# Kernel optimization log

Measured on AMD Instinct MI355X. Metric: run time of the kernel, lower is better.

The kernel has to match this reference:

```python
import jax, jax.numpy as jnp
import numpy as np

N_NODES = 50000
N_EDGES = 800000
IN_CH = 128
OUT_CH = 64
HEADS = 4
NEG_SLOPE = 0.2  # PyG GATConv default


def setup_inputs() -> dict:
    key = jax.random.key(0)
    k1, k2, k3, k4, k5 = jax.random.split(key, 5)
    x = jax.random.normal(k1, (N_NODES, IN_CH), dtype=jnp.float32)
    edge_index = jax.random.randint(k2, (2, N_EDGES), 0, N_NODES, dtype=jnp.int64)
    W = jax.random.normal(k3, (HEADS * OUT_CH, IN_CH), dtype=jnp.float32) * (1.0 / np.sqrt(IN_CH))
    att_src = jax.random.normal(k4, (HEADS, OUT_CH), dtype=jnp.float32) * (1.0 / np.sqrt(OUT_CH))
    att_dst = jax.random.normal(k5, (HEADS, OUT_CH), dtype=jnp.float32) * (1.0 / np.sqrt(OUT_CH))
    bias = jnp.zeros((OUT_CH,), dtype=jnp.float32)
    return {"x": x, "edge_index": edge_index, "W": W,
            "att_src": att_src, "att_dst": att_dst, "bias": bias}


def reference(x, edge_index, W, att_src, att_dst, bias):
    # GAT2NO_NORM.forward in eval mode: dropout == identity.
    N = x.shape[0]
    H, C = att_src.shape
    # PyG GATConv adds self-loops by default.
    loop = jnp.arange(N, dtype=edge_index.dtype)
    src = jnp.concatenate([edge_index[0], loop])  # message source j
    dst = jnp.concatenate([edge_index[1], loop])  # message target i
    # Linear projection, reshape to heads: [N, H, C]
    h = (x @ W.T).reshape(N, H, C)
    # Per-node attention halves: [N, H]
    a_src = jnp.einsum('nhc,hc->nh', h, att_src)
    a_dst = jnp.einsum('nhc,hc->nh', h, att_dst)
    # Per-edge raw score, LeakyReLU: [E, H]
    e = jax.nn.leaky_relu(a_src[src] + a_dst[dst], NEG_SLOPE)
    # Segment (edge-)softmax over incoming edges of each dst node.
    m = jax.lax.stop_gradient(jax.ops.segment_max(e, dst, num_segments=N))
    ex = jnp.exp(e - m[dst])
    denom = jax.ops.segment_sum(ex, dst, num_segments=N)
    alpha = ex / denom[dst]  # self-loops guarantee denom > 0
    # Weighted scatter-sum of messages: [N, H, C]
    msg = h[src] * alpha[:, :, None]
    out = jax.ops.segment_sum(msg, dst, num_segments=N)
    # concat=False -> mean over heads, then bias, then ReLU (module wrapper)
    out = out.mean(axis=1) + bias
    return jax.nn.relu(out)
```

## Files before the change

### kernel.cpp

```cpp
#include <hip/hip_runtime.h>
#include <hip/hip_fp16.h>
#include <math.h>

#define N_NODES 50000
#define N_EDGES 800000
#define IN_CH 128
#define PROJ_CH 256
#define OUT_CH 64
#define HEADS 4
#define NEG_SLOPE 0.2f
#define CAP 80
#define PROJ_BLOCKS 782
#define GRID_BLOCKS 3125

typedef _Float16 f16x8 __attribute__((ext_vector_type(8)));
typedef _Float16 f16x4 __attribute__((ext_vector_type(4)));
typedef __fp16   hf2   __attribute__((ext_vector_type(2)));
typedef float    f32x4 __attribute__((ext_vector_type(4)));

__device__ __forceinline__ float leaky(float v) {
    return v > 0.f ? v : NEG_SLOPE * v;
}

__device__ __forceinline__ hf2 u32_as_h2(unsigned int u) {
    union { unsigned int u; hf2 h; } c; c.u = u; return c.h;
}

__global__ __launch_bounds__(256) void mega_kernel(
    const float* __restrict__ x, const float* __restrict__ W,
    const float* __restrict__ att_src, const float* __restrict__ att_dst,
    const int* __restrict__ ei, int* __restrict__ cnt, unsigned short* __restrict__ csr,
    _Float16* __restrict__ h, float* __restrict__ a_src, float* __restrict__ a_dst)
{
    __shared__ _Float16 xs[64 * 136];
    const int tid = threadIdx.x;
    const int bid = blockIdx.x;

    const int e = bid * 256 + tid;
    const int esrc = ei[e];
    const int edst = ei[N_EDGES + e];

    if (bid >= PROJ_BLOCKS) {
        int pos = atomicAdd(&cnt[edst], 1);
        if (pos < CAP) csr[edst * CAP + pos] = (unsigned short)esrc;
        return;
    }

    const int w    = tid >> 6;
    const int lane = tid & 63;
    const int q    = lane >> 4;
    const int l15  = lane & 15;
    const int nb   = bid * 64;

    f16x8 B[4][4];
#pragma unroll
    for (int k0i = 0; k0i < 4; ++k0i)
#pragma unroll
        for (int n0i = 0; n0i < 4; ++n0i) {
            const int oc = w * 64 + n0i * 16 + l15;
            const float* src = W + (size_t)oc * IN_CH + k0i * 32 + q * 8;
            float4 s0 = *(const float4*)src;
            float4 s1 = *(const float4*)(src + 4);
            f16x8 v;
            v[0] = (_Float16)s0.x; v[1] = (_Float16)s0.y;
            v[2] = (_Float16)s0.z; v[3] = (_Float16)s0.w;
            v[4] = (_Float16)s1.x; v[5] = (_Float16)s1.y;
            v[6] = (_Float16)s1.z; v[7] = (_Float16)s1.w;
            B[k0i][n0i] = v;
        }

#pragma unroll
    for (int r = 0; r < 8; ++r) {
        int v   = r * 256 + tid;
        int row = v >> 5;
        int c4  = v & 31;
        int grow = nb + row;
        if (grow > N_NODES - 1) grow = N_NODES - 1;
        float4 xv = *(const float4*)(x + (size_t)grow * IN_CH + c4 * 4);
        f16x4 hv;
        hv[0] = (_Float16)xv.x; hv[1] = (_Float16)xv.y;
        hv[2] = (_Float16)xv.z; hv[3] = (_Float16)xv.w;
        *(f16x4*)&xs[row * 136 + c4 * 4] = hv;
    }
    __syncthreads();

    const int pos = atomicAdd(&cnt[edst], 1);

    f32x4 acc[4][4];
#pragma unroll
    for (int m0i = 0; m0i < 4; ++m0i)
#pragma unroll
        for (int n0i = 0; n0i < 4; ++n0i)
            acc[m0i][n0i] = (f32x4){0.f, 0.f, 0.f, 0.f};

#pragma unroll
    for (int k0i = 0; k0i < 4; ++k0i) {
        f16x8 A[4];
#pragma unroll
        for (int m0i = 0; m0i < 4; ++m0i)
            A[m0i] = *(const f16x8*)&xs[(m0i * 16 + l15) * 136 + k0i * 32 + q * 8];
#pragma unroll
        for (int n0i = 0; n0i < 4; ++n0i)
#pragma unroll
            for (int m0i = 0; m0i < 4; ++m0i)
                acc[m0i][n0i] = __builtin_amdgcn_mfma_f32_16x16x32_f16(
                    A[m0i], B[k0i][n0i], acc[m0i][n0i], 0, 0, 0);
    }

    float att_s[4], att_d[4];
#pragma unroll
    for (int n0i = 0; n0i < 4; ++n0i) {
        att_s[n0i] = att_src[w * 64 + n0i * 16 + l15];
        att_d[n0i] = att_dst[w * 64 + n0i * 16 + l15];
    }

#pragma unroll
    for (int m0i = 0; m0i < 4; ++m0i) {
        float vs[4], vd[4];
#pragma unroll
        for (int r = 0; r < 4; ++r) {
            float s = 0.f, d = 0.f;
#pragma unroll
            for (int n0i = 0; n0i < 4; ++n0i) {
                s = fmaf(acc[m0i][n0i][r], att_s[n0i], s);
                d = fmaf(acc[m0i][n0i][r], att_d[n0i], d);
            }
            vs[r] = s; vd[r] = d;
        }
#pragma unroll
        for (int off = 1; off < 16; off <<= 1) {
#pragma unroll
            for (int r = 0; r < 4; ++r) {
                vs[r] += __shfl_xor(vs[r], off, 64);
                vd[r] += __shfl_xor(vd[r], off, 64);
            }
        }
#pragma unroll
        for (int r = 0; r < 4; ++r) {
            int node = nb + m0i * 16 + q * 4 + r;
            if (l15 == 0 && node < N_NODES) {
                a_src[node * HEADS + w] = vs[r];
                a_dst[node * HEADS + w] = vd[r];
            }
        }
#pragma unroll
        for (int r = 0; r < 4; ++r) {
            int node = nb + m0i * 16 + q * 4 + r;
            if (node < N_NODES) {
#pragma unroll
                for (int n0i = 0; n0i < 4; ++n0i)
                    h[(size_t)node * PROJ_CH + w * 64 + n0i * 16 + l15] =
                        (_Float16)acc[m0i][n0i][r];
            }
        }
    }

    if (pos < CAP) csr[edst * CAP + pos] = (unsigned short)esrc;
}

__global__ __launch_bounds__(256) void aggregate_kernel(
    const _Float16* __restrict__ h, const float* __restrict__ a_src,
    const float* __restrict__ a_dst, const int* __restrict__ cnt,
    const unsigned short* __restrict__ csr, const float* __restrict__ bias,
    float* __restrict__ out)
{
    const int tid  = threadIdx.x;
    const int wave = tid >> 6;
    const int l    = tid & 63;
    const int i    = blockIdx.x * 4 + wave;

    __shared__ float lw_all[4][(CAP + 1) * 4];
    __shared__ int   lj_all[4][CAP + 4];
    float* lw = lw_all[wave];
    int*   lj = lj_all[wave];

    const int n    = min(cnt[i], CAP);
    const int base = i * CAP;
    const int h4   = l & 3;
    const float adh = a_dst[i * 4 + h4];

    float lsum = 0.f;
    {
        float ws = __expf(leaky(a_src[i * 4 + h4] + adh));
        if (l < 4) { lw[l] = ws; lsum = ws; }
        if (l == 0) lj[0] = i;
    }

    const int erel = l >> 2;
    for (int p0 = 0; p0 < n; p0 += 16) {
        int e = p0 + erel;
        bool valid = e < n;
        int j = valid ? (int)csr[base + e] : 0;
        float w = 0.f;
        if (valid) w = __expf(leaky(a_src[j * 4 + h4] + adh));
        lsum += w;
        lw[(e + 1) * 4 + h4] = w;
        if (h4 == 0) lj[e + 1] = j;
    }
#pragma unroll
    for (int off = 4; off < 64; off <<= 1) lsum += __shfl_xor(lsum, off, 64);

    __syncthreads();

    const int half_ = l >> 5;
    const int jj    = l & 31;
    const int hd    = jj >> 3;
    const int m_total = n + 1;
    const uint4* hv = (const uint4*)h;

    float acc[8];
#pragma unroll
    for (int k = 0; k < 8; ++k) acc[k] = 0.f;

    for (int qq = 0; qq < m_total; qq += 8) {
        const int eb = qq + 4 * half_;
        int ia[4]; float wa[4];
#pragma unroll
        for (int k = 0; k < 4; ++k) {
            int e = eb + k;
            ia[k] = (e < m_total) ? e : 0;
            wa[k] = (e < m_total) ? lw[ia[k] * 4 + hd] : 0.f;
        }
        uint4 d0 = hv[(size_t)lj[ia[0]] * 32 + jj];
        uint4 d1 = hv[(size_t)lj[ia[1]] * 32 + jj];
        uint4 d2 = hv[(size_t)lj[ia[2]] * 32 + jj];
        uint4 d3 = hv[(size_t)lj[ia[3]] * 32 + jj];
        hf2 wab = __builtin_amdgcn_cvt_pkrtz(wa[0], wa[1]);
        hf2 wcd = __builtin_amdgcn_cvt_pkrtz(wa[2], wa[3]);

        const unsigned int* A0 = (const unsigned int*)&d0;
        const unsigned int* A1 = (const unsigned int*)&d1;
        const unsigned int* A2 = (const unsigned int*)&d2;
        const unsigned int* A3 = (const unsigned int*)&d3;
#pragma unroll
        for (int k = 0; k < 4; ++k) {
            unsigned int lo01 = __builtin_amdgcn_perm(A1[k], A0[k], 0x05040100u);
            unsigned int hi01 = __builtin_amdgcn_perm(A1[k], A0[k], 0x07060302u);
            acc[2 * k]     = __builtin_amdgcn_fdot2(u32_as_h2(lo01), wab, acc[2 * k], false);
            acc[2 * k + 1] = __builtin_amdgcn_fdot2(u32_as_h2(hi01), wab, acc[2 * k + 1], false);
            unsigned int lo23 = __builtin_amdgcn_perm(A3[k], A2[k], 0x05040100u);
            unsigned int hi23 = __builtin_amdgcn_perm(A3[k], A2[k], 0x07060302u);
            acc[2 * k]     = __builtin_amdgcn_fdot2(u32_as_h2(lo23), wcd, acc[2 * k], false);
            acc[2 * k + 1] = __builtin_amdgcn_fdot2(u32_as_h2(hi23), wcd, acc[2 * k + 1], false);
        }
    }

#pragma unroll
    for (int k = 0; k < 8; ++k) acc[k] += __shfl_xor(acc[k], 32, 64);

    float linv = 1.f / __shfl(lsum, hd, 64);
#pragma unroll
    for (int k = 0; k < 8; ++k) {
        float r = acc[k] * linv;
        r += __shfl_xor(r, 8, 64);
        r += __shfl_xor(r, 16, 64);
        acc[k] = r;
    }

    if (l < 8) {
        float* op = out + (size_t)i * OUT_CH + l * 8;
        float4 o0, o1;
        o0.x = fmaxf(0.25f * acc[0] + bias[l * 8 + 0], 0.f);
        o0.y = fmaxf(0.25f * acc[1] + bias[l * 8 + 1], 0.f);
        o0.z = fmaxf(0.25f * acc[2] + bias[l * 8 + 2], 0.f);
        o0.w = fmaxf(0.25f * acc[3] + bias[l * 8 + 3], 0.f);
        o1.x = fmaxf(0.25f * acc[4] + bias[l * 8 + 4], 0.f);
        o1.y = fmaxf(0.25f * acc[5] + bias[l * 8 + 5], 0.f);
        o1.z = fmaxf(0.25f * acc[6] + bias[l * 8 + 6], 0.f);
        o1.w = fmaxf(0.25f * acc[7] + bias[l * 8 + 7], 0.f);
        *(float4*)op = o0;
        *((float4*)op + 1) = o1;
    }
}

extern "C" void kernel_launch(void* const* d_in, const int* in_sizes, int n_in,
                              void* d_out, int out_size, void* d_ws, size_t ws_size,
                              hipStream_t stream)
{
    const float* x       = (const float*)d_in[0];
    const int*   ei      = (const int*)d_in[1];
    const float* W       = (const float*)d_in[2];
    const float* att_src = (const float*)d_in[3];
    const float* att_dst = (const float*)d_in[4];
    const float* bias    = (const float*)d_in[5];
    float* out = (float*)d_out;

    _Float16* h   = (_Float16*)d_ws;
    float* asrc  = (float*)(h + (size_t)N_NODES * PROJ_CH);
    float* adst  = asrc + (size_t)N_NODES * HEADS;
    int*   cnt   = (int*)(adst + (size_t)N_NODES * HEADS);
    unsigned short* csr = (unsigned short*)(cnt + N_NODES);

    (void)hipMemsetAsync(cnt, 0, N_NODES * sizeof(int), stream);
    hipLaunchKernelGGL(mega_kernel, dim3(GRID_BLOCKS), dim3(256), 0, stream,
                       x, W, att_src, att_dst, ei, cnt, csr, h, asrc, adst);
    hipLaunchKernelGGL(aggregate_kernel, dim3(N_NODES / 4), dim3(256), 0, stream,
                       h, asrc, adst, cnt, csr, bias, out);
}
```

Measured before the change: 198.6 us.

## Pre-convert W to fp16, stage h stores through LDS, widen aggregate gather batch

Adds a prep kernel that converts W to fp16 once and zeroes the counters, replacing the memset and the per-block fp32 W loads and conversions. The projection now issues x loads before the W loads. The edge atomic is moved to the start of the kernel so it overlaps the GEMM. The output h is staged through LDS so each node row is written with coalesced 16-byte stores instead of scattered 2-byte stores. The aggregation loop gathers 8 neighbor rows per half-wave per iteration instead of 4, raising memory-level parallelism at the cost of more registers and an extra kernel launch.

```diff
diff --git a/kernel.cpp b/kernel.cpp
--- a/kernel.cpp
+++ b/kernel.cpp
@@ -26,8 +26,16 @@
     union { unsigned int u; hf2 h; } c; c.u = u; return c.h;
 }
 
+__global__ __launch_bounds__(256) void prep_kernel(
+    const float* __restrict__ W, _Float16* __restrict__ Wh, int* __restrict__ cnt)
+{
+    const int t = blockIdx.x * 256 + threadIdx.x;
+    if (t < PROJ_CH * IN_CH) Wh[t] = (_Float16)W[t];
+    if (t < N_NODES) cnt[t] = 0;
+}
+
 __global__ __launch_bounds__(256) void mega_kernel(
-    const float* __restrict__ x, const float* __restrict__ W,
+    const float* __restrict__ x, const _Float16* __restrict__ Wh,
     const float* __restrict__ att_src, const float* __restrict__ att_dst,
     const int* __restrict__ ei, int* __restrict__ cnt, unsigned short* __restrict__ csr,
     _Float16* __restrict__ h, float* __restrict__ a_src, float* __restrict__ a_dst)
@@ -39,9 +47,9 @@
     const int e = bid * 256 + tid;
     const int esrc = ei[e];
     const int edst = ei[N_EDGES + e];
+    const int pos = atomicAdd(&cnt[edst], 1);
 
     if (bid >= PROJ_BLOCKS) {
-        int pos = atomicAdd(&cnt[edst], 1);
         if (pos < CAP) csr[edst * CAP + pos] = (unsigned short)esrc;
         return;
     }
@@ -52,23 +60,7 @@
     const int l15  = lane & 15;
     const int nb   = bid * 64;
 
-    f16x8 B[4][4];
-#pragma unroll
-    for (int k0i = 0; k0i < 4; ++k0i)
-#pragma unroll
-        for (int n0i = 0; n0i < 4; ++n0i) {
-            const int oc = w * 64 + n0i * 16 + l15;
-            const float* src = W + (size_t)oc * IN_CH + k0i * 32 + q * 8;
-            float4 s0 = *(const float4*)src;
-            float4 s1 = *(const float4*)(src + 4);
-            f16x8 v;
-            v[0] = (_Float16)s0.x; v[1] = (_Float16)s0.y;
-            v[2] = (_Float16)s0.z; v[3] = (_Float16)s0.w;
-            v[4] = (_Float16)s1.x; v[5] = (_Float16)s1.y;
-            v[6] = (_Float16)s1.z; v[7] = (_Float16)s1.w;
-            B[k0i][n0i] = v;
-        }
-
+    float4 xv[8];
 #pragma unroll
     for (int r = 0; r < 8; ++r) {
         int v   = r * 256 + tid;
@@ -76,15 +68,29 @@
         int c4  = v & 31;
         int grow = nb + row;
         if (grow > N_NODES - 1) grow = N_NODES - 1;
-        float4 xv = *(const float4*)(x + (size_t)grow * IN_CH + c4 * 4);
+        xv[r] = *(const float4*)(x + (size_t)grow * IN_CH + c4 * 4);
+    }
+
+    f16x8 B[4][4];
+#pragma unroll
+    for (int k0i = 0; k0i < 4; ++k0i)
+#pragma unroll
+        for (int n0i = 0; n0i < 4; ++n0i) {
+            const int oc = w * 64 + n0i * 16 + l15;
+            B[k0i][n0i] = *(const f16x8*)(Wh + (size_t)oc * IN_CH + k0i * 32 + q * 8);
+        }
+
+#pragma unroll
+    for (int r = 0; r < 8; ++r) {
+        int v   = r * 256 + tid;
+        int row = v >> 5;
+        int c4  = v & 31;
         f16x4 hv;
-        hv[0] = (_Float16)xv.x; hv[1] = (_Float16)xv.y;
-        hv[2] = (_Float16)xv.z; hv[3] = (_Float16)xv.w;
+        hv[0] = (_Float16)xv[r].x; hv[1] = (_Float16)xv[r].y;
+        hv[2] = (_Float16)xv[r].z; hv[3] = (_Float16)xv[r].w;
         *(f16x4*)&xs[row * 136 + c4 * 4] = hv;
     }
     __syncthreads();
-
-    const int pos = atomicAdd(&cnt[edst], 1);
 
     f32x4 acc[4][4];
 #pragma unroll
@@ -143,16 +149,38 @@
                 a_dst[node * HEADS + w] = vd[r];
             }
         }
+    }
+
+    unsigned char* lb = (unsigned char*)xs;
+    __syncthreads();
+#pragma unroll
+    for (int p = 0; p < 2; ++p) {
+#pragma unroll
+        for (int mm = 0; mm < 2; ++mm) {
+            const int m0i = 2 * p + mm;
+            const int nl0 = mm * 16 + q * 4;
+#pragma unroll
+            for (int n0i = 0; n0i < 4; ++n0i) {
+                const int ch = w * 64 + n0i * 16 + l15;
+#pragma unroll
+                for (int r = 0; r < 4; ++r)
+                    *(_Float16*)(lb + (nl0 + r) * 528 + ch * 2) =
+                        (_Float16)acc[m0i][n0i][r];
+            }
+        }
+        __syncthreads();
 #pragma unroll
         for (int r = 0; r < 4; ++r) {
-            int node = nb + m0i * 16 + q * 4 + r;
+            int idx  = r * 256 + tid;
+            int nl   = idx >> 5;
+            int ck   = idx & 31;
+            int node = nb + p * 32 + nl;
             if (node < N_NODES) {
-#pragma unroll
-                for (int n0i = 0; n0i < 4; ++n0i)
-                    h[(size_t)node * PROJ_CH + w * 64 + n0i * 16 + l15] =
-                        (_Float16)acc[m0i][n0i][r];
-            }
-        }
+                f16x8 vv = *(const f16x8*)(lb + nl * 528 + ck * 16);
+                *(f16x8*)(h + (size_t)node * PROJ_CH + ck * 8) = vv;
+            }
+        }
+        if (p == 0) __syncthreads();
     }
 
     if (pos < CAP) csr[edst * CAP + pos] = (unsigned short)esrc;
@@ -212,36 +240,37 @@
 #pragma unroll
     for (int k = 0; k < 8; ++k) acc[k] = 0.f;
 
-    for (int qq = 0; qq < m_total; qq += 8) {
-        const int eb = qq + 4 * half_;
-        int ia[4]; float wa[4];
-#pragma unroll
-        for (int k = 0; k < 4; ++k) {
-            int e = eb + k;
-            ia[k] = (e < m_total) ? e : 0;
-            wa[k] = (e < m_total) ? lw[ia[k] * 4 + hd] : 0.f;
-        }
-        uint4 d0 = hv[(size_t)lj[ia[0]] * 32 + jj];
-        uint4 d1 = hv[(size_t)lj[ia[1]] * 32 + jj];
-        uint4 d2 = hv[(size_t)lj[ia[2]] * 32 + jj];
-        uint4 d3 = hv[(size_t)lj[ia[3]] * 32 + jj];
-        hf2 wab = __builtin_amdgcn_cvt_pkrtz(wa[0], wa[1]);
-        hf2 wcd = __builtin_amdgcn_cvt_pkrtz(wa[2], wa[3]);
-
-        const unsigned int* A0 = (const unsigned int*)&d0;
-        const unsigned int* A1 = (const unsigned int*)&d1;
-        const unsigned int* A2 = (const unsigned int*)&d2;
-        const unsigned int* A3 = (const unsigned int*)&d3;
-#pragma unroll
-        for (int k = 0; k < 4; ++k) {
-            unsigned int lo01 = __builtin_amdgcn_perm(A1[k], A0[k], 0x05040100u);
-            unsigned int hi01 = __builtin_amdgcn_perm(A1[k], A0[k], 0x07060302u);
-            acc[2 * k]     = __builtin_amdgcn_fdot2(u32_as_h2(lo01), wab, acc[2 * k], false);
-            acc[2 * k + 1] = __builtin_amdgcn_fdot2(u32_as_h2(hi01), wab, acc[2 * k + 1], false);
-            unsigned int lo23 = __builtin_amdgcn_perm(A3[k], A2[k], 0x05040100u);
-            unsigned int hi23 = __builtin_amdgcn_perm(A3[k], A2[k], 0x07060302u);
-            acc[2 * k]     = __builtin_amdgcn_fdot2(u32_as_h2(lo23), wcd, acc[2 * k], false);
-            acc[2 * k + 1] = __builtin_amdgcn_fdot2(u32_as_h2(hi23), wcd, acc[2 * k + 1], false);
+    for (int qq = 0; qq < m_total; qq += 16) {
+        const int eb = qq + 8 * half_;
+        int ia[8]; float wa[8];
+#pragma unroll
+        for (int k = 0; k < 8; ++k) {
+            int e2 = eb + k;
+            bool v = e2 < m_total;
+            ia[k] = v ? e2 : 0;
+            wa[k] = v ? lw[ia[k] * 4 + hd] : 0.f;
+        }
+        uint4 d[8];
+#pragma unroll
+        for (int k = 0; k < 8; ++k)
+            d[k] = hv[(size_t)lj[ia[k]] * 32 + jj];
+
+        hf2 wp[4];
+#pragma unroll
+        for (int pr = 0; pr < 4; ++pr)
+            wp[pr] = __builtin_amdgcn_cvt_pkrtz(wa[2 * pr], wa[2 * pr + 1]);
+
+#pragma unroll
+        for (int pr = 0; pr < 4; ++pr) {
+            const unsigned int* Aa = (const unsigned int*)&d[2 * pr];
+            const unsigned int* Ab = (const unsigned int*)&d[2 * pr + 1];
+#pragma unroll
+            for (int k = 0; k < 4; ++k) {
+                unsigned int lo = __builtin_amdgcn_perm(Ab[k], Aa[k], 0x05040100u);
+                unsigned int hi = __builtin_amdgcn_perm(Ab[k], Aa[k], 0x07060302u);
+                acc[2 * k]     = __builtin_amdgcn_fdot2(u32_as_h2(lo), wp[pr], acc[2 * k], false);
+                acc[2 * k + 1] = __builtin_amdgcn_fdot2(u32_as_h2(hi), wp[pr], acc[2 * k + 1], false);
+            }
         }
     }
 
@@ -290,10 +319,11 @@
     float* adst  = asrc + (size_t)N_NODES * HEADS;
     int*   cnt   = (int*)(adst + (size_t)N_NODES * HEADS);
     unsigned short* csr = (unsigned short*)(cnt + N_NODES);
-
-    (void)hipMemsetAsync(cnt, 0, N_NODES * sizeof(int), stream);
+    _Float16* Wh = (_Float16*)(csr + (size_t)N_NODES * CAP);
+
+    hipLaunchKernelGGL(prep_kernel, dim3(196), dim3(256), 0, stream, W, Wh, cnt);
     hipLaunchKernelGGL(mega_kernel, dim3(GRID_BLOCKS), dim3(256), 0, stream,
-                       x, W, att_src, att_dst, ei, cnt, csr, h, asrc, adst);
+                       x, Wh, att_src, att_dst, ei, cnt, csr, h, asrc, adst);
     hipLaunchKernelGGL(aggregate_kernel, dim3(N_NODES / 4), dim3(256), 0, stream,
                        h, asrc, adst, cnt, csr, bias, out);
 }
```

New measurement: 205.6 us. 3.5% more time.
